# Optimization experiments

Measured on AMD Instinct MI355X. Metric: run time of the kernel, lower is better.

The kernel has to match this reference:

```python
import jax, jax.numpy as jnp
import numpy as np

# Model config (matches init_kwargs)
E, TOP_K, H, I = 16, 2, 2048, 1024
B, S = 2, 2048
GROUP = 16                 # NVFP4 quantization group size along contraction dim
RSF = 1.0                  # routed_scaling_factor


def setup_inputs() -> dict:
    key = jax.random.key(0)
    ks = jax.random.split(key, 6)
    hidden_states = jax.random.normal(ks[0], (B, S, H), dtype=jnp.float32)
    gate_weight = jax.random.normal(ks[1], (E, H), dtype=jnp.float32) * 0.02
    # int4 codes stored as int32 in [0,16); reference subtracts 8 -> [-8,7]
    fc_up_qweights = jax.random.randint(ks[2], (E, H, I), 0, 16, dtype=jnp.int32)
    fc_up_blocks_scale = jax.random.uniform(ks[3], (E, H // GROUP, I), dtype=jnp.float32) * 0.02
    fc_up_global_scale = jnp.ones((1,), dtype=jnp.float32)
    fc_down_qweights = jax.random.randint(ks[4], (E, I, H), 0, 16, dtype=jnp.int32)
    fc_down_blocks_scale = jax.random.uniform(ks[5], (E, I // GROUP, H), dtype=jnp.float32) * 0.02
    fc_down_global_scale = jnp.ones((1,), dtype=jnp.float32)
    return {
        'hidden_states': hidden_states,
        'gate_weight': gate_weight,
        'fc_up_blocks_scale': fc_up_blocks_scale,
        'fc_up_global_scale': fc_up_global_scale,
        'fc_down_blocks_scale': fc_down_blocks_scale,
        'fc_down_global_scale': fc_down_global_scale,
        'fc_up_qweights': fc_up_qweights,
        'fc_down_qweights': fc_down_qweights,
    }


def _dequant(q, blocks_scale, global_scale):
    # q: [E,K,N] int codes (0..15 -> -8..7); blocks_scale: [E,K/GROUP,N]
    e, k, n = q.shape
    w = (q.astype(jnp.float32) - 8.0).reshape(e, k // GROUP, GROUP, n)
    w = w * blocks_scale[:, :, None, :]
    return w.reshape(e, k, n) * global_scale[0]


def reference(hidden_states, gate_weight, fc_up_blocks_scale, fc_up_global_scale,
              fc_down_blocks_scale, fc_down_global_scale,
              fc_up_qweights, fc_down_qweights):
    b, s, h = hidden_states.shape
    x = hidden_states.reshape(-1, h).astype(jnp.float32)          # [T,H]
    t = x.shape[0]

    # Router: HF sigmoid routing mapped through logsigmoid so that
    # softmax(logsigmoid(l)) == sigmoid(l)/sum(sigmoid(l))  (nemotron_h_plugin_router_logits)
    logits = jax.nn.log_sigmoid(x @ gate_weight.T)                # [T,E]
    probs = jax.nn.softmax(logits, axis=-1)
    topw, topi = jax.lax.top_k(probs, TOP_K)                      # [T,K]
    topw = topw / (jnp.sum(topw, axis=-1, keepdims=True) + 1e-20) # renormalize

    # Dense per-token expert weights [T,E] (scatter of top-k weights)
    wdense = jnp.zeros((t, E), dtype=jnp.float32)
    wdense = wdense.at[jnp.arange(t)[:, None], topi].add(topw) * RSF

    w_up = _dequant(fc_up_qweights, fc_up_blocks_scale, fc_up_global_scale)     # [E,H,I]
    w_down = _dequant(fc_down_qweights, fc_down_blocks_scale, fc_down_global_scale)  # [E,I,H]

    z = jnp.einsum('th,ehi->tei', x, w_up)                        # up proj
    a = jnp.square(jnp.maximum(z, 0.0))                           # activation_type=0: ReLU^2
    aw = a * wdense[:, :, None]                                   # fold routing weights (linear)
    y = jnp.einsum('tei,eih->th', aw, w_down)                     # down proj + combine
    return y.reshape(b, s, h)
```

## Files before the change

kernel.cpp:

```cpp
#include <hip/hip_runtime.h>

#define TOK 4096
#define NE 16
#define HD 2048
#define ID 1024
#define QGROUP 16
#define CAP 4096

typedef _Float16 half4v __attribute__((ext_vector_type(4)));
typedef _Float16 half8v __attribute__((ext_vector_type(8)));
typedef float float4v __attribute__((ext_vector_type(4)));

__device__ __forceinline__ void g2l16(const void* g, void* l) {
    __builtin_amdgcn_global_load_lds(
        (const __attribute__((address_space(1))) unsigned int*)g,
        (__attribute__((address_space(3))) unsigned int*)l, 16, 0, 0);
}

__global__ __launch_bounds__(256) void router_kernel(
    const float* __restrict__ x, const float* __restrict__ gw,
    _Float16* __restrict__ xh, int* __restrict__ topi, float* __restrict__ topw)
{
    const int t = blockIdx.x;
    const int tid = threadIdx.x;
    const int h8 = tid * 8;
    const float* xr = x + (size_t)t * HD;
    const float4 f0 = *(const float4*)&xr[h8];
    const float4 f1 = *(const float4*)&xr[h8 + 4];
    half8v hv;
    hv[0] = (_Float16)f0.x; hv[1] = (_Float16)f0.y; hv[2] = (_Float16)f0.z; hv[3] = (_Float16)f0.w;
    hv[4] = (_Float16)f1.x; hv[5] = (_Float16)f1.y; hv[6] = (_Float16)f1.z; hv[7] = (_Float16)f1.w;
    *(half8v*)&xh[(size_t)t * HD + h8] = hv;

    float p[NE];
#pragma unroll
    for (int e = 0; e < NE; e++) {
        const float4 g0 = *(const float4*)&gw[e * HD + h8];
        const float4 g1 = *(const float4*)&gw[e * HD + h8 + 4];
        p[e] = f0.x * g0.x + f0.y * g0.y + f0.z * g0.z + f0.w * g0.w
             + f1.x * g1.x + f1.y * g1.y + f1.z * g1.z + f1.w * g1.w;
    }
#pragma unroll
    for (int off = 32; off > 0; off >>= 1) {
#pragma unroll
        for (int e = 0; e < NE; e++) p[e] += __shfl_down(p[e], off, 64);
    }
    __shared__ float part[4][NE];
    int wave = tid >> 6, lane = tid & 63;
    if (lane == 0) {
#pragma unroll
        for (int e = 0; e < NE; e++) part[wave][e] = p[e];
    }
    __syncthreads();
    if (tid == 0) {
        float s[NE]; float sum = 0.f;
#pragma unroll
        for (int e = 0; e < NE; e++) {
            float l = part[0][e] + part[1][e] + part[2][e] + part[3][e];
            float sg = 1.f / (1.f + expf(-l));
            s[e] = sg; sum += sg;
        }
        int i1 = 0;
#pragma unroll
        for (int e = 1; e < NE; e++) if (s[e] > s[i1]) i1 = e;
        int i2 = (i1 == 0) ? 1 : 0;
#pragma unroll
        for (int e = 0; e < NE; e++) if (e != i1 && s[e] > s[i2]) i2 = e;
        float p1 = s[i1] / sum, p2 = s[i2] / sum;
        float inv = 1.f / (p1 + p2 + 1e-20f);
        topi[t * 2 + 0] = i1; topw[t * 2 + 0] = p1 * inv;
        topi[t * 2 + 1] = i2; topw[t * 2 + 1] = p2 * inv;
    }
}

__global__ __launch_bounds__(256) void compact_kernel(
    const int* __restrict__ topi, const float* __restrict__ topw,
    int* __restrict__ counts, int* __restrict__ pair_row, float* __restrict__ pair_w)
{
    const int e = blockIdx.x;
    const int tid = threadIdx.x;
    const int lane = tid & 63, wv = tid >> 6;
    __shared__ int wsum[4];
    int running = 0;
    for (int base = 0; base < 2 * TOK; base += 256) {
        const int idx = base + tid;
        const bool f = (topi[idx] == e);
        unsigned long long b = __ballot(f);
        int pre = __popcll(b & ((1ull << lane) - 1ull));
        if (lane == 0) wsum[wv] = __popcll(b);
        __syncthreads();
        int woff = 0;
#pragma unroll
        for (int w = 0; w < 4; w++) if (w < wv) woff += wsum[w];
        const int tot = wsum[0] + wsum[1] + wsum[2] + wsum[3];
        if (f) {
            const int pos = running + woff + pre;
            pair_row[e * CAP + pos] = idx;
            pair_w[e * CAP + pos] = topw[idx];
        }
        running += tot;
        __syncthreads();
    }
    if (tid == 0) counts[e] = running;
}

template<int K, int N>
__global__ __launch_bounds__(256) void dequantT_kernel(
    const int* __restrict__ qw, const float* __restrict__ bsc, _Float16* __restrict__ wq)
{
    const int e = blockIdx.z, kt = blockIdx.y, nt = blockIdx.x;
    const int tid = threadIdx.x;
    __shared__ _Float16 T[64][68];

    const int c4 = (tid & 15) * 4;
    const int r0 = tid >> 4;
#pragma unroll
    for (int p = 0; p < 4; p++) {
        const int r = p * 16 + r0;
        const int kabs = kt * 64 + r;
        const int4 c = *(const int4*)&qw[((size_t)e * K + kabs) * N + nt * 64 + c4];
        const float4 sc = *(const float4*)&bsc[((size_t)e * (K / QGROUP) + (kabs >> 4)) * N + nt * 64 + c4];
        half4v h;
        h[0] = (_Float16)((float)(c.x - 8) * sc.x);
        h[1] = (_Float16)((float)(c.y - 8) * sc.y);
        h[2] = (_Float16)((float)(c.z - 8) * sc.z);
        h[3] = (_Float16)((float)(c.w - 8) * sc.w);
        *(half4v*)&T[r][c4] = h;
    }
    __syncthreads();
    const int nrow = tid >> 2;
    const int kseg = (tid & 3) * 16;
    half8v o0, o1;
#pragma unroll
    for (int i = 0; i < 8; i++) o0[i] = T[kseg + i][nrow];
#pragma unroll
    for (int i = 0; i < 8; i++) o1[i] = T[kseg + 8 + i][nrow];
    _Float16* dst = wq + ((size_t)e * N + nt * 64 + nrow) * K + kt * 64 + kseg;
    *(half8v*)dst = o0;
    *(half8v*)(dst + 8) = o1;
}

template<int N, int K, bool UP>
__global__ __launch_bounds__(256, 3) void gemm5_kernel(
    const _Float16* __restrict__ A, const _Float16* __restrict__ BT,
    const float* __restrict__ gsc,
    const int* __restrict__ counts, const int* __restrict__ pair_row,
    const float* __restrict__ pair_w,
    _Float16* __restrict__ store16, float* __restrict__ store32)
{
    constexpr int NT = N / 128;
    constexpr int MT = CAP / 64;
    constexpr int NK = K / 64;
    const int bx = blockIdx.x;
    const int g8 = bx & 7;
    const int rest = bx >> 3;
    const int m = rest % MT;
    const int g = (rest / MT) * 8 + g8;
    const int e = g / NT, nt = g % NT;
    const int cnt = counts[e];
    const int mbase = m * 64;
    if (mbase >= cnt) return;
    const int nbase = nt * 128;
    const int tid = threadIdx.x;

    __shared__ _Float16 As[2][64 * 64];
    __shared__ _Float16 Bs[2][128 * 64];
    __shared__ int rows_s[64];
    __shared__ float pw_s[64];

    if (tid < 64) {
        int idx = mbase + tid; if (idx >= cnt) idx = cnt - 1;
        rows_s[tid] = pair_row[e * CAP + idx];
        pw_s[tid] = UP ? pair_w[e * CAP + idx] : 0.f;
    }
    __syncthreads();

    const _Float16* asrc[2]; int aoff[2];
#pragma unroll
    for (int j = 0; j < 2; j++) {
        const int gidx = j * 256 + tid;
        const int r = gidx >> 3, s = gidx & 7, c = s ^ (r & 7);
        const int pr = rows_s[r];
        asrc[j] = A + (size_t)(UP ? (pr >> 1) : pr) * K + c * 8;
        aoff[j] = r * 64 + s * 8;
    }
    const _Float16* bsrc[4]; int boff[4];
#pragma unroll
    for (int j = 0; j < 4; j++) {
        const int gidx = j * 256 + tid;
        const int r = gidx >> 3, s = gidx & 7, c = s ^ (r & 7);
        bsrc[j] = BT + ((size_t)e * N + nbase + r) * K + c * 8;
        boff[j] = r * 64 + s * 8;
    }

    const int lane = tid & 63, wv = tid >> 6;
    const int quad = lane >> 4, lm = lane & 15;
    const int wm = (wv & 1) * 32, wn = (wv >> 1) * 64;

    float4v acc[2][4];
#pragma unroll
    for (int mi = 0; mi < 2; mi++)
#pragma unroll
        for (int ni = 0; ni < 4; ni++) acc[mi][ni] = (float4v){0.f, 0.f, 0.f, 0.f};

#pragma unroll
    for (int j = 0; j < 2; j++) g2l16(asrc[j], &As[0][aoff[j]]);
#pragma unroll
    for (int j = 0; j < 4; j++) g2l16(bsrc[j], &Bs[0][boff[j]]);
#pragma unroll
    for (int j = 0; j < 2; j++) g2l16(asrc[j] + 64, &As[1][aoff[j]]);
#pragma unroll
    for (int j = 0; j < 4; j++) g2l16(bsrc[j] + 64, &Bs[1][boff[j]]);

    for (int it = 0; it < NK; ++it) {
        if (it + 1 < NK) {
            asm volatile("s_waitcnt vmcnt(6)" ::: "memory");
        } else {
            asm volatile("s_waitcnt vmcnt(0)" ::: "memory");
        }
        __builtin_amdgcn_s_barrier();
        asm volatile("" ::: "memory");
        const int cur = it & 1;
#pragma unroll
        for (int ks = 0; ks < 2; ks++) {
            half8v af[2], bf[4];
#pragma unroll
            for (int mi = 0; mi < 2; mi++) {
                const int r = wm + mi * 16 + lm;
                const int s = (ks * 4 + quad) ^ (r & 7);
                af[mi] = *(const half8v*)&As[cur][r * 64 + s * 8];
            }
#pragma unroll
            for (int ni = 0; ni < 4; ni++) {
                const int r = wn + ni * 16 + lm;
                const int s = (ks * 4 + quad) ^ (r & 7);
                bf[ni] = *(const half8v*)&Bs[cur][r * 64 + s * 8];
            }
#pragma unroll
            for (int mi = 0; mi < 2; mi++)
#pragma unroll
                for (int ni = 0; ni < 4; ni++)
                    acc[mi][ni] = __builtin_amdgcn_mfma_f32_16x16x32_f16(af[mi], bf[ni], acc[mi][ni], 0, 0, 0);
        }
        asm volatile("" ::: "memory");
        __builtin_amdgcn_s_barrier();
        asm volatile("" ::: "memory");
        if (it + 2 < NK) {
            const int k0n = (it + 2) * 64;
#pragma unroll
            for (int j = 0; j < 2; j++) g2l16(asrc[j] + k0n, &As[cur][aoff[j]]);
#pragma unroll
            for (int j = 0; j < 4; j++) g2l16(bsrc[j] + k0n, &Bs[cur][boff[j]]);
        }
    }

    const float gs = gsc[0];
#pragma unroll
    for (int mi = 0; mi < 2; mi++) {
#pragma unroll
        for (int r = 0; r < 4; r++) {
            const int rl = wm + mi * 16 + quad * 4 + r;
            if (mbase + rl < cnt) {
                const int pr = rows_s[rl];
#pragma unroll
                for (int ni = 0; ni < 4; ni++) {
                    const int col = nbase + wn + ni * 16 + lm;
                    float v = acc[mi][ni][r] * gs;
                    if (UP) {
                        v = fmaxf(v, 0.f);
                        v = v * v * pw_s[rl];
                        store16[(size_t)pr * N + col] = (_Float16)v;
                    } else if (store16) {
                        store16[(size_t)pr * N + col] = (_Float16)v;
                    } else {
                        atomicAdd(&store32[(size_t)(pr >> 1) * N + col], v);
                    }
                }
            }
        }
    }
}

__global__ __launch_bounds__(256) void combine_kernel(
    const _Float16* __restrict__ part, float* __restrict__ out)
{
    const size_t i8 = ((size_t)blockIdx.x * 256 + threadIdx.x) * 8;
    const size_t t = i8 >> 11;
    const int h = (int)(i8 & (HD - 1));
    const half8v a = *(const half8v*)&part[(t * 2) * HD + h];
    const half8v b = *(const half8v*)&part[(t * 2 + 1) * HD + h];
    float4 o0, o1;
    o0.x = (float)a[0] + (float)b[0];
    o0.y = (float)a[1] + (float)b[1];
    o0.z = (float)a[2] + (float)b[2];
    o0.w = (float)a[3] + (float)b[3];
    o1.x = (float)a[4] + (float)b[4];
    o1.y = (float)a[5] + (float)b[5];
    o1.z = (float)a[6] + (float)b[6];
    o1.w = (float)a[7] + (float)b[7];
    *(float4*)&out[i8] = o0;
    *(float4*)&out[i8 + 4] = o1;
}

template<int N, int K, bool UP>
__global__ __launch_bounds__(256) void gemm_fused_kernel(
    const _Float16* __restrict__ A, const int* __restrict__ qw,
    const float* __restrict__ bsc, const float* __restrict__ gsc,
    const int* __restrict__ counts, const int* __restrict__ pair_row,
    const float* __restrict__ pair_w,
    _Float16* __restrict__ store16, float* __restrict__ store32)
{
    constexpr int NT = N / 128;
    const int e = blockIdx.y;
    const int cnt = counts[e];
    const int mt = blockIdx.x / NT, nt = blockIdx.x % NT;
    const int mbase = mt * 128;
    if (mbase >= cnt) return;
    const int nbase = nt * 128;
    const int tid = threadIdx.x;

    __shared__ _Float16 As[128][40];
    __shared__ _Float16 Bs[128][40];
    __shared__ int rows_s[128];
    __shared__ float pw_s[128];

    if (tid < 128) {
        int idx = mbase + tid; if (idx >= cnt) idx = cnt - 1;
        rows_s[tid] = pair_row[e * CAP + idx];
        pw_s[tid] = UP ? pair_w[e * CAP + idx] : 0.f;
    }

    const int lane = tid & 63, wv = tid >> 6;
    const int quad = lane >> 4, lm = lane & 15;
    const int wr = (wv >> 1) * 64, wc = (wv & 1) * 64;

    float4v acc[4][4];
#pragma unroll
    for (int mi = 0; mi < 4; mi++)
#pragma unroll
        for (int ni = 0; ni < 4; ni++) acc[mi][ni] = (float4v){0.f, 0.f, 0.f, 0.f};

    const int am = tid & 127, akk = (tid >> 7) * 16;
    const int bn4 = (tid & 31) * 4, bkb = (tid >> 5) * 4;

    for (int k0 = 0; k0 < K; k0 += 32) {
        __syncthreads();
        {
            int pr = rows_s[am];
            const _Float16* src = A + (size_t)(UP ? (pr >> 1) : pr) * K + k0 + akk;
            *(uint4*)&As[am][akk] = *(const uint4*)src;
            *(uint4*)&As[am][akk + 8] = *(const uint4*)(src + 8);
        }
        {
            const int kabs = k0 + bkb;
            const float4 sc = *(const float4*)&bsc[((size_t)e * (K / QGROUP) + (kabs >> 4)) * N + nbase + bn4];
            const int4 c0 = *(const int4*)&qw[((size_t)e * K + kabs + 0) * N + nbase + bn4];
            const int4 c1 = *(const int4*)&qw[((size_t)e * K + kabs + 1) * N + nbase + bn4];
            const int4 c2 = *(const int4*)&qw[((size_t)e * K + kabs + 2) * N + nbase + bn4];
            const int4 c3 = *(const int4*)&qw[((size_t)e * K + kabs + 3) * N + nbase + bn4];
            half4v q;
            q[0] = (_Float16)((c0.x - 8) * sc.x); q[1] = (_Float16)((c1.x - 8) * sc.x);
            q[2] = (_Float16)((c2.x - 8) * sc.x); q[3] = (_Float16)((c3.x - 8) * sc.x);
            *(half4v*)&Bs[bn4 + 0][bkb] = q;
            q[0] = (_Float16)((c0.y - 8) * sc.y); q[1] = (_Float16)((c1.y - 8) * sc.y);
            q[2] = (_Float16)((c2.y - 8) * sc.y); q[3] = (_Float16)((c3.y - 8) * sc.y);
            *(half4v*)&Bs[bn4 + 1][bkb] = q;
            q[0] = (_Float16)((c0.z - 8) * sc.z); q[1] = (_Float16)((c1.z - 8) * sc.z);
            q[2] = (_Float16)((c2.z - 8) * sc.z); q[3] = (_Float16)((c3.z - 8) * sc.z);
            *(half4v*)&Bs[bn4 + 2][bkb] = q;
            q[0] = (_Float16)((c0.w - 8) * sc.w); q[1] = (_Float16)((c1.w - 8) * sc.w);
            q[2] = (_Float16)((c2.w - 8) * sc.w); q[3] = (_Float16)((c3.w - 8) * sc.w);
            *(half4v*)&Bs[bn4 + 3][bkb] = q;
        }
        __syncthreads();
        half8v af[4], bf[4];
#pragma unroll
        for (int mi = 0; mi < 4; mi++)
            af[mi] = *(const half8v*)&As[wr + mi * 16 + lm][quad * 8];
#pragma unroll
        for (int ni = 0; ni < 4; ni++)
            bf[ni] = *(const half8v*)&Bs[wc + ni * 16 + lm][quad * 8];
#pragma unroll
        for (int mi = 0; mi < 4; mi++)
#pragma unroll
            for (int ni = 0; ni < 4; ni++)
                acc[mi][ni] = __builtin_amdgcn_mfma_f32_16x16x32_f16(af[mi], bf[ni], acc[mi][ni], 0, 0, 0);
    }

    const float gs = gsc[0];
#pragma unroll
    for (int mi = 0; mi < 4; mi++) {
#pragma unroll
        for (int r = 0; r < 4; r++) {
            const int rl = wr + mi * 16 + quad * 4 + r;
            if (mbase + rl < cnt) {
                const int pr = rows_s[rl];
#pragma unroll
                for (int ni = 0; ni < 4; ni++) {
                    const int col = nbase + wc + ni * 16 + lm;
                    float v = acc[mi][ni][r] * gs;
                    if (UP) {
                        v = fmaxf(v, 0.f);
                        v = v * v * pw_s[rl];
                        store16[(size_t)pr * N + col] = (_Float16)v;
                    } else {
                        atomicAdd(&store32[(size_t)(pr >> 1) * N + col], v);
                    }
                }
            }
        }
    }
}

extern "C" void kernel_launch(void* const* d_in, const int* in_sizes, int n_in,
                              void* d_out, int out_size, void* d_ws, size_t ws_size,
                              hipStream_t stream) {
    const float* x   = (const float*)d_in[0];
    const float* gw  = (const float*)d_in[1];
    const float* usc = (const float*)d_in[2];
    const float* ugs = (const float*)d_in[3];
    const float* dsc = (const float*)d_in[4];
    const float* dgs = (const float*)d_in[5];
    const int*   uq  = (const int*)d_in[6];
    const int*   dq  = (const int*)d_in[7];
    float* out = (float*)d_out;

    char* ws = (char*)d_ws;
    int*   counts   = (int*)(ws + 0);
    int*   pair_row = (int*)(ws + 4096);
    float* pair_w   = (float*)(ws + 4096 + (size_t)NE * CAP * 4);
    _Float16* xh    = (_Float16*)(ws + 528384);
    _Float16* act   = (_Float16*)(ws + 528384 + (size_t)TOK * HD * 2);
    _Float16* wq    = (_Float16*)(ws + 528384 + (size_t)TOK * HD * 2
                                  + (size_t)2 * TOK * ID * 2);
    int*   topi = (int*)wq;
    float* topw = (float*)((char*)wq + (size_t)2 * TOK * 4);
    const size_t deq_end = 34082816ull + (size_t)NE * HD * ID * 2;
    const bool use_deq = ws_size >= deq_end;
    _Float16* part = (_Float16*)(ws + deq_end);
    const bool use_part = use_deq && (ws_size >= deq_end + (size_t)2 * TOK * HD * 2);

    if (!use_part)
        hipMemsetAsync(out, 0, (size_t)TOK * HD * 4, stream);

    router_kernel<<<TOK, 256, 0, stream>>>(x, gw, xh, topi, topw);
    compact_kernel<<<NE, 256, 0, stream>>>(topi, topw, counts, pair_row, pair_w);

    if (use_deq) {
        dequantT_kernel<HD, ID><<<dim3(ID / 64, HD / 64, NE), 256, 0, stream>>>(uq, usc, wq);
        gemm5_kernel<ID, HD, true><<<(CAP / 64) * (ID / 128) * NE, 256, 0, stream>>>(
            xh, wq, ugs, counts, pair_row, pair_w, act, nullptr);
        dequantT_kernel<ID, HD><<<dim3(HD / 64, ID / 64, NE), 256, 0, stream>>>(dq, dsc, wq);
        gemm5_kernel<HD, ID, false><<<(CAP / 64) * (HD / 128) * NE, 256, 0, stream>>>(
            act, wq, dgs, counts, pair_row, pair_w, use_part ? part : nullptr, out);
        if (use_part)
            combine_kernel<<<(TOK * HD) / (256 * 8), 256, 0, stream>>>(part, out);
    } else {
        gemm_fused_kernel<ID, HD, true><<<dim3((CAP / 128) * (ID / 128), NE), 256, 0, stream>>>(
            xh, uq, usc, ugs, counts, pair_row, pair_w, act, nullptr);
        gemm_fused_kernel<HD, ID, false><<<dim3((CAP / 128) * (HD / 128), NE), 256, 0, stream>>>(
            act, dq, dsc, dgs, counts, pair_row, pair_w, nullptr, out);
    }
}
```

Measured before the change: 525.7 us.

## Triple-buffer LDS tiles in the expert GEMM and repad the dequant transpose tile

The grouped expert GEMM moves from a two-stage to a three-stage LDS ring, keeping two K-tiles of async global-to-LDS loads in flight, with a new wait-count schedule and a peeled tail. The extra LDS per block forces the launch-bounds occupancy hint down from 3 to 2 blocks per CU. The aim is to hide more global load latency, at the cost of fewer resident waves. The dequant transpose tile's row padding changes from 68 to 70 halves, with 32-bit split stores, to change LDS bank conflicts on the column reads.

```diff
diff --git a/kernel.cpp b/kernel.cpp
--- a/kernel.cpp
+++ b/kernel.cpp
@@ -110,7 +110,7 @@
 {
     const int e = blockIdx.z, kt = blockIdx.y, nt = blockIdx.x;
     const int tid = threadIdx.x;
-    __shared__ _Float16 T[64][68];
+    __shared__ _Float16 T[64][70];
 
     const int c4 = (tid & 15) * 4;
     const int r0 = tid >> 4;
@@ -120,12 +120,13 @@
         const int kabs = kt * 64 + r;
         const int4 c = *(const int4*)&qw[((size_t)e * K + kabs) * N + nt * 64 + c4];
         const float4 sc = *(const float4*)&bsc[((size_t)e * (K / QGROUP) + (kabs >> 4)) * N + nt * 64 + c4];
-        half4v h;
-        h[0] = (_Float16)((float)(c.x - 8) * sc.x);
-        h[1] = (_Float16)((float)(c.y - 8) * sc.y);
-        h[2] = (_Float16)((float)(c.z - 8) * sc.z);
-        h[3] = (_Float16)((float)(c.w - 8) * sc.w);
-        *(half4v*)&T[r][c4] = h;
+        union { _Float16 h[4]; unsigned u[2]; } cv;
+        cv.h[0] = (_Float16)((float)(c.x - 8) * sc.x);
+        cv.h[1] = (_Float16)((float)(c.y - 8) * sc.y);
+        cv.h[2] = (_Float16)((float)(c.z - 8) * sc.z);
+        cv.h[3] = (_Float16)((float)(c.w - 8) * sc.w);
+        *(unsigned*)&T[r][c4]     = cv.u[0];
+        *(unsigned*)&T[r][c4 + 2] = cv.u[1];
     }
     __syncthreads();
     const int nrow = tid >> 2;
@@ -141,7 +142,7 @@
 }
 
 template<int N, int K, bool UP>
-__global__ __launch_bounds__(256, 3) void gemm5_kernel(
+__global__ __launch_bounds__(256, 2) void gemm5_kernel(
     const _Float16* __restrict__ A, const _Float16* __restrict__ BT,
     const float* __restrict__ gsc,
     const int* __restrict__ counts, const int* __restrict__ pair_row,
@@ -163,8 +164,8 @@
     const int nbase = nt * 128;
     const int tid = threadIdx.x;
 
-    __shared__ _Float16 As[2][64 * 64];
-    __shared__ _Float16 Bs[2][128 * 64];
+    __shared__ _Float16 As[3][64 * 64];
+    __shared__ _Float16 Bs[3][128 * 64];
     __shared__ int rows_s[64];
     __shared__ float pw_s[64];
 
@@ -204,23 +205,14 @@
         for (int ni = 0; ni < 4; ni++) acc[mi][ni] = (float4v){0.f, 0.f, 0.f, 0.f};
 
 #pragma unroll
-    for (int j = 0; j < 2; j++) g2l16(asrc[j], &As[0][aoff[j]]);
-#pragma unroll
-    for (int j = 0; j < 4; j++) g2l16(bsrc[j], &Bs[0][boff[j]]);
-#pragma unroll
-    for (int j = 0; j < 2; j++) g2l16(asrc[j] + 64, &As[1][aoff[j]]);
-#pragma unroll
-    for (int j = 0; j < 4; j++) g2l16(bsrc[j] + 64, &Bs[1][boff[j]]);
-
-    for (int it = 0; it < NK; ++it) {
-        if (it + 1 < NK) {
-            asm volatile("s_waitcnt vmcnt(6)" ::: "memory");
-        } else {
-            asm volatile("s_waitcnt vmcnt(0)" ::: "memory");
-        }
-        __builtin_amdgcn_s_barrier();
-        asm volatile("" ::: "memory");
-        const int cur = it & 1;
+    for (int q = 0; q < 3; q++) {
+#pragma unroll
+        for (int j = 0; j < 2; j++) g2l16(asrc[j] + q * 64, &As[q][aoff[j]]);
+#pragma unroll
+        for (int j = 0; j < 4; j++) g2l16(bsrc[j] + q * 64, &Bs[q][boff[j]]);
+    }
+
+    auto compute = [&](int cur) {
 #pragma unroll
         for (int ks = 0; ks < 2; ks++) {
             half8v af[2], bf[4];
@@ -242,17 +234,38 @@
                 for (int ni = 0; ni < 4; ni++)
                     acc[mi][ni] = __builtin_amdgcn_mfma_f32_16x16x32_f16(af[mi], bf[ni], acc[mi][ni], 0, 0, 0);
         }
+    };
+
+    int cur = 0;
+    for (int it = 0; it < NK - 2; ++it) {
+        asm volatile("s_waitcnt vmcnt(12)" ::: "memory");
+        __builtin_amdgcn_s_barrier();
+        asm volatile("" ::: "memory");
+        compute(cur);
         asm volatile("" ::: "memory");
         __builtin_amdgcn_s_barrier();
         asm volatile("" ::: "memory");
-        if (it + 2 < NK) {
-            const int k0n = (it + 2) * 64;
+        if (it + 3 < NK) {
+            const int k0n = (it + 3) * 64;
 #pragma unroll
             for (int j = 0; j < 2; j++) g2l16(asrc[j] + k0n, &As[cur][aoff[j]]);
 #pragma unroll
             for (int j = 0; j < 4; j++) g2l16(bsrc[j] + k0n, &Bs[cur][boff[j]]);
         }
-    }
+        cur = (cur == 2) ? 0 : cur + 1;
+    }
+    asm volatile("s_waitcnt vmcnt(6)" ::: "memory");
+    __builtin_amdgcn_s_barrier();
+    asm volatile("" ::: "memory");
+    compute(cur);
+    asm volatile("" ::: "memory");
+    __builtin_amdgcn_s_barrier();
+    asm volatile("" ::: "memory");
+    cur = (cur == 2) ? 0 : cur + 1;
+    asm volatile("s_waitcnt vmcnt(0)" ::: "memory");
+    __builtin_amdgcn_s_barrier();
+    asm volatile("" ::: "memory");
+    compute(cur);
 
     const float gs = gsc[0];
 #pragma unroll
```

Result: no change. 536.0 us (+2.0%).
